# Optimization experiments

Hardware: AMD Instinct MI355X
Metric: run time of the kernel (lower is better)

## Reference

```python
import jax, jax.numpy as jnp
import numpy as np

K = 8
B = 3.0
DIM = 32
HID = 32
BATCH = 65536
MIN_BW = 1e-3
MIN_BH = 1e-3
MIN_D = 1e-3


def setup_inputs() -> dict:
    key = jax.random.key(0)
    ks = jax.random.split(key, 8)
    L = DIM - 1
    x = jax.random.normal(ks[0], (BATCH, DIM), jnp.float32)
    init_param = jax.random.uniform(ks[1], (3 * K - 1,), jnp.float32, -0.5, 0.5)
    # stacked per-dim FCNN weights; layer l conditions on x[:, :l+1] -> causal zero-mask
    w1 = jax.random.normal(ks[2], (L, L, HID), jnp.float32) * 0.2
    mask = (jnp.arange(L)[None, :] <= jnp.arange(L)[:, None]).astype(jnp.float32)
    w1 = w1 * mask[:, :, None]
    b1 = jax.random.normal(ks[3], (L, HID), jnp.float32) * 0.1
    w2 = jax.random.normal(ks[4], (L, HID, HID), jnp.float32) * 0.2
    b2 = jax.random.normal(ks[5], (L, HID), jnp.float32) * 0.1
    w3 = jax.random.normal(ks[6], (L, HID, 3 * K - 1), jnp.float32) * 0.2
    b3 = jax.random.normal(ks[7], (L, 3 * K - 1), jnp.float32) * 0.1
    return {"x": x, "init_param": init_param, "w1": w1, "b1": b1,
            "w2": w2, "b2": b2, "w3": w3, "b3": b3}


def _rqs_forward(x, Wu, Hu, Du):
    # x: [dim, batch]; Wu, Hu: [dim, batch, K]; Du: [dim, batch, K-1]
    inside = (x >= -B) & (x <= B)
    xc = jnp.clip(x, -B, B)
    # bin widths
    widths = jax.nn.softmax(Wu, axis=-1)
    widths = MIN_BW + (1.0 - MIN_BW * K) * widths
    cw = jnp.cumsum(widths, axis=-1)
    cw = jnp.concatenate([jnp.zeros(cw.shape[:-1] + (1,), cw.dtype), cw], axis=-1)
    cw = 2.0 * B * cw - B
    cw = cw.at[..., 0].set(-B).at[..., -1].set(B)
    widths = cw[..., 1:] - cw[..., :-1]
    # bin heights
    heights = jax.nn.softmax(Hu, axis=-1)
    heights = MIN_BH + (1.0 - MIN_BH * K) * heights
    ch = jnp.cumsum(heights, axis=-1)
    ch = jnp.concatenate([jnp.zeros(ch.shape[:-1] + (1,), ch.dtype), ch], axis=-1)
    ch = 2.0 * B * ch - B
    ch = ch.at[..., 0].set(-B).at[..., -1].set(B)
    heights = ch[..., 1:] - ch[..., :-1]
    # knot derivatives, edges pinned so softplus(const)+min_d = 1
    const = float(np.log(np.exp(1.0 - MIN_D) - 1.0))
    pad = jnp.full(Du.shape[:-1] + (1,), const, Du.dtype)
    derivs = MIN_D + jax.nn.softplus(jnp.concatenate([pad, Du, pad], axis=-1))  # [.., K+1]
    # bin search (searchsorted on cumwidths, eps bump on last edge)
    cw_s = cw.at[..., -1].add(1e-6)
    idx = jnp.sum((xc[..., None] >= cw_s).astype(jnp.int32), axis=-1) - 1
    idx = jnp.clip(idx, 0, K - 1)
    g = lambda a: jnp.take_along_axis(a, idx[..., None], axis=-1)[..., 0]
    in_cw = g(cw)
    in_w = g(widths)
    in_ch = g(ch)
    in_h = g(heights)
    in_delta = g(heights / widths)
    d0 = g(derivs)
    d1 = g(derivs[..., 1:])
    theta = (xc - in_cw) / in_w
    tt = theta * (1.0 - theta)
    num = in_h * (in_delta * theta ** 2 + d0 * tt)
    den = in_delta + (d0 + d1 - 2.0 * in_delta) * tt
    out = in_ch + num / den
    dnum = in_delta ** 2 * (d1 * theta ** 2 + 2.0 * in_delta * tt + d0 * (1.0 - theta) ** 2)
    ld = jnp.log(dnum) - 2.0 * jnp.log(den)
    out = jnp.where(inside, out, x)  # identity tails
    ld = jnp.where(inside, ld, 0.0)
    return out, ld


def reference(x, init_param, w1, b1, w2, b2, w3, b3):
    # all per-dim conditioners at once (w1 is causally masked in setup)
    h1 = jnp.tanh(jnp.einsum('bd,ldh->lbh', x[:, :DIM - 1], w1) + b1[:, None, :])
    h2 = jnp.tanh(jnp.einsum('lbh,lhg->lbg', h1, w2) + b2[:, None, :])
    out = jnp.einsum('lbh,lho->lbo', h2, w3) + b3[:, None, :]  # [dim-1, batch, 3K-1]
    p0 = jnp.broadcast_to(init_param, (1, x.shape[0], 3 * K - 1))
    params = jnp.concatenate([p0, out], axis=0)  # [dim, batch, 3K-1]
    Wu = 2.0 * B * jax.nn.softmax(params[..., :K], axis=-1)
    Hu = 2.0 * B * jax.nn.softmax(params[..., K:2 * K], axis=-1)
    Du = jax.nn.softplus(params[..., 2 * K:])
    z_t, ld = _rqs_forward(x.T, Wu, Hu, Du)  # [dim, batch]
    return z_t.T, jnp.sum(ld, axis=0)
```

## Files before the change

### kernel.cpp

```cpp
#include <hip/hip_runtime.h>
#include <hip/hip_bf16.h>
#include <cmath>

constexpr int KN   = 8;
constexpr int NPAR = 23;
constexpr int DD   = 32;
constexpr float BND   = 3.0f;
constexpr float MINBW = 1e-3f;
constexpr float MIND  = 1e-3f;

#define TPB   256
#define ROWS  256
#define GDIMS 4
#define WST   40
#define PSTH  24
#define RECB  8192

typedef __attribute__((ext_vector_type(8))) short short8;
typedef __attribute__((ext_vector_type(4))) float float4v;
typedef __attribute__((ext_vector_type(2))) __fp16 fp16x2;
typedef __attribute__((ext_vector_type(8))) _Float16 half8v;

#define RCP(x) __builtin_amdgcn_rcpf(x)

__device__ __forceinline__ short f2bf(float f) {
    unsigned u = __float_as_uint(f);
    u += 0x7fffu + ((u >> 16) & 1u);
    return (short)(u >> 16);
}

__device__ __forceinline__ int pkbf(float a, float b) {
    union { __hip_bfloat162 v; int i; } u;
    u.v = __float22bfloat162_rn(make_float2(a, b));
    return u.i;
}

__device__ __forceinline__ int pkh(float a, float b) {
    union { fp16x2 h; int i; } u;
    u.h = __builtin_amdgcn_cvt_pkrtz(a, b);
    return u.i;
}

__device__ __forceinline__ float fast_tanh(float x) {
    float e = __expf(2.0f * x);
    return 1.0f - 2.0f * RCP(e + 1.0f);
}

__device__ __forceinline__ float softplus_fast(float v) {
    return __logf(1.0f + __expf(v));
}

__device__ __forceinline__ float rqs_apply(float xv, const float* p, float& ldout) {
    float cw[KN + 1], ch[KN + 1];
    {
        float t0[KN]; float s = 0.f;
#pragma unroll
        for (int k = 0; k < KN; ++k) { t0[k] = __expf(p[k]); s += t0[k]; }
        float inv = (2.0f * BND) * RCP(s);
        float e2[KN]; float s2 = 0.f;
#pragma unroll
        for (int k = 0; k < KN; ++k) { e2[k] = __expf(inv * t0[k]); s2 += e2[k]; }
        float fac = (1.0f - MINBW * KN) * RCP(s2);
        float c = 0.f;
        cw[0] = -BND;
#pragma unroll
        for (int k = 0; k < KN; ++k) { c += MINBW + fac * e2[k]; cw[k + 1] = 2.0f * BND * c - BND; }
        cw[KN] = BND;
    }
    {
        float t0[KN]; float s = 0.f;
#pragma unroll
        for (int k = 0; k < KN; ++k) { t0[k] = __expf(p[KN + k]); s += t0[k]; }
        float inv = (2.0f * BND) * RCP(s);
        float e2[KN]; float s2 = 0.f;
#pragma unroll
        for (int k = 0; k < KN; ++k) { e2[k] = __expf(inv * t0[k]); s2 += e2[k]; }
        float fac = (1.0f - MINBW * KN) * RCP(s2);
        float c = 0.f;
        ch[0] = -BND;
#pragma unroll
        for (int k = 0; k < KN; ++k) { c += MINBW + fac * e2[k]; ch[k + 1] = 2.0f * BND * c - BND; }
        ch[KN] = BND;
    }

    float xc = fminf(fmaxf(xv, -BND), BND);
    float in_cw = cw[0], in_w = cw[1] - cw[0];
    float in_ch = ch[0], in_h = ch[1] - ch[0];
    float dl0 = 0.0f, dl1 = p[2 * KN];
    bool e0 = true, e1 = false;
#pragma unroll
    for (int k = 1; k < KN; ++k) {
        bool c = (xc >= cw[k]);
        in_cw = c ? cw[k]            : in_cw;
        in_w  = c ? (cw[k+1]-cw[k])  : in_w;
        in_ch = c ? ch[k]            : in_ch;
        in_h  = c ? (ch[k+1]-ch[k])  : in_h;
        dl0   = c ? p[2*KN + k - 1]  : dl0;
        if (k < KN - 1) dl1 = c ? p[2*KN + k] : dl1;
        if (k == 1)      e0 = !c;
        if (k == KN - 1) e1 = c;
    }
    float d0 = e0 ? 1.0f : (MIND + softplus_fast(softplus_fast(dl0)));
    float d1 = e1 ? 1.0f : (MIND + softplus_fast(softplus_fast(dl1)));

    float rw    = RCP(in_w);
    float th    = (xc - in_cw) * rw;
    float delta = in_h * rw;
    float tt    = th * (1.0f - th);
    float th2   = th * th;
    float num   = in_h * (delta * th2 + d0 * tt);
    float den   = delta + (d0 + d1 - 2.0f * delta) * tt;
    float z     = in_ch + num * RCP(den);
    float omt   = 1.0f - th;
    float dnum  = delta * delta * (d1 * th2 + 2.0f * delta * tt + d0 * omt * omt);
    float ldv   = __logf(dnum) - 2.0f * __logf(den);

    bool inside = (xv >= -BND) && (xv <= BND);
    ldout = inside ? ldv : 0.0f;
    return inside ? z : xv;
}

__device__ __forceinline__ short8 xpose_h(float4v cA, float4v cB,
                                          float4 bA, float4 bB,
                                          int odd, int sl_a, int sl_b, bool qlow) {
    int a0 = pkbf(fast_tanh(cA[0] + bA.x), fast_tanh(cA[1] + bA.y));
    int a1 = pkbf(fast_tanh(cA[2] + bA.z), fast_tanh(cA[3] + bA.w));
    int b0 = pkbf(fast_tanh(cB[0] + bB.x), fast_tanh(cB[1] + bB.y));
    int b1 = pkbf(fast_tanh(cB[2] + bB.z), fast_tanh(cB[3] + bB.w));
    int p0 = odd ? b0 : a0, p1 = odd ? b1 : a1;
    int p2 = odd ? a0 : b0, p3 = odd ? a1 : b1;
    int g0 = __shfl(p0, sl_a, 64);
    int g1 = __shfl(p1, sl_a, 64);
    int g2 = __shfl(p2, sl_b, 64);
    int g3 = __shfl(p3, sl_b, 64);
    union { int4 i; short8 s; } u;
    u.i = qlow ? make_int4(g0, g1, g2, g3) : make_int4(g2, g3, g0, g1);
    return u.s;
}

extern "C" __global__ void __launch_bounds__(256)
k_prep(const float* __restrict__ w1, const float* __restrict__ b1,
       const float* __restrict__ w2, const float* __restrict__ b2,
       const float* __restrict__ w3, const float* __restrict__ b3,
       char* __restrict__ wbuf, float* __restrict__ ldo, int B)
{
    const int l = blockIdx.x, tid = threadIdx.x;
    if (l >= 31) {
        const int zb = l - 31;
        const int chunk = B >> 6;
        float4* dst = (float4*)(ldo + (size_t)zb * chunk);
        for (int i = tid; i < (chunk >> 2); i += 256)
            dst[i] = make_float4(0.f, 0.f, 0.f, 0.f);
        return;
    }
    short* r1 = (short*)(wbuf + (size_t)l * RECB);
    short* r2 = r1 + 1280;
    short* r3 = r2 + 1280;
    float* f1 = (float*)(wbuf + (size_t)l * RECB + 7680);
    float* f2 = f1 + 32;
    float* f3 = f2 + 32;
    const float* g1 = w1 + (size_t)l * 992;
    const float* g2 = w2 + (size_t)l * 1024;
    const float* g3 = w3 + (size_t)l * 736;
    for (int i = tid; i < 1280; i += 256) {
        int n = i / WST, k = i - WST * n;
        r1[i] = (k < 31) ? f2bf(g1[k * 32 + n]) : (short)0;
        r2[i] = (k < 32) ? f2bf(g2[k * 32 + n]) : (short)0;
        r3[i] = (n < 23 && k < 32) ? f2bf(g3[k * 23 + n]) : (short)0;
    }
    if (tid < 32) { f1[tid] = b1[(size_t)l * 32 + tid]; f2[tid] = b2[(size_t)l * 32 + tid]; }
    if (tid < 32) f3[tid] = (tid < 23) ? b3[(size_t)l * 23 + tid] : 0.0f;
}

extern "C" __global__ void __launch_bounds__(TPB, 5)
k_nsf(const float* __restrict__ x,
      const float* __restrict__ p0,
      const char* __restrict__ wbuf,
      float* __restrict__ zo, float* __restrict__ ldo, int B)
{
    __shared__ __align__(16) char sRec[RECB];
    __shared__ __align__(16) _Float16 sP[ROWS * PSTH];

    const short* sW1 = (const short*)sRec;
    const short* sW2 = sW1 + 1280;
    const short* sW3 = sW1 + 2560;
    const float* sB1 = (const float*)(sRec + 7680);
    const float* sB2 = sB1 + 32;
    const float* sB3 = sB1 + 64;

    const int tid  = threadIdx.x;
    const int lane = tid & 63;
    const int wv   = tid >> 6;
    const int q    = lane >> 4;
    const int ln   = lane & 15;
    const int qb   = q & 1;
    const bool qlow = (q < 2);
    const int s_even = ln + 32 * qb;
    const int s_odd  = s_even + 16;
    const int sl_a = qlow ? s_even : s_odd;
    const int sl_b = qlow ? s_odd  : s_even;
    const int g    = blockIdx.y;
    const int ly0  = GDIMS * g;
    const long long rowbase = (long long)blockIdx.x * ROWS;
    const long long row = rowbase + tid;

    float xarr[GDIMS];
    {
        float4 xs = *(const float4*)(x + row * DD + ly0);
        xarr[0] = xs.x; xarr[1] = xs.y; xarr[2] = xs.z; xarr[3] = xs.w;
    }

    float zreg[GDIMS];
    float ldacc = 0.0f;

#pragma unroll
    for (int j = 0; j < GDIMS; ++j) {
        const int ly = ly0 + j;
        if (ly == 0) {
            float pr[NPAR];
#pragma unroll
            for (int k = 0; k < NPAR; ++k) pr[k] = p0[k];
            float ld;
            zreg[0] = rqs_apply(xarr[0], pr, ld);
            ldacc += ld;
            continue;
        }
        const int l = ly - 1;

        {
            const int4* src = (const int4*)(wbuf + (size_t)l * RECB);
            int4* dst = (int4*)sRec;
            dst[tid]       = src[tid];
            dst[tid + 256] = src[tid + 256];
        }
        __syncthreads();

        short8 w1a = *(const short8*)&sW1[ln * WST + q * 8];
        short8 w1b = *(const short8*)&sW1[(16 + ln) * WST + q * 8];
        short8 w2a = *(const short8*)&sW2[ln * WST + q * 8];
        short8 w2b = *(const short8*)&sW2[(16 + ln) * WST + q * 8];
        short8 w3a = *(const short8*)&sW3[ln * WST + q * 8];
        short8 w3b = *(const short8*)&sW3[(16 + ln) * WST + q * 8];
        float4 bA1 = *(const float4*)&sB1[4 * q];
        float4 bB1 = *(const float4*)&sB1[16 + 4 * q];
        float4 bA2 = *(const float4*)&sB2[4 * q];
        float4 bB2 = *(const float4*)&sB2[16 + 4 * q];
        float4 bA3 = *(const float4*)&sB3[4 * q];
        float4 bB3 = *(const float4*)&sB3[16 + 4 * q];

        short8 au[4];
#pragma unroll
        for (int t = 0; t < 4; ++t) {
            const int m0 = 64 * wv + 16 * t;
            const float4* xp = (const float4*)(x + (rowbase + m0 + ln) * DD + q * 8);
            float4 uu = xp[0], vv = xp[1];
            union { int4 i; short8 s; } c;
            c.i = make_int4(pkbf(uu.x, uu.y), pkbf(uu.z, uu.w),
                            pkbf(vv.x, vv.y), pkbf(vv.z, vv.w));
            au[t] = c.s;
        }
        float4v cA[4], cB[4];
#pragma unroll
        for (int t = 0; t < 4; ++t) {
            float4v zz = {0.f,0.f,0.f,0.f};
            cA[t] = __builtin_amdgcn_mfma_f32_16x16x32_bf16(w1a, au[t], zz, 0, 0, 0);
            cB[t] = __builtin_amdgcn_mfma_f32_16x16x32_bf16(w1b, au[t], zz, 0, 0, 0);
        }
        short8 h1f[4];
#pragma unroll
        for (int t = 0; t < 4; ++t)
            h1f[t] = xpose_h(cA[t], cB[t], bA1, bB1, qb, sl_a, sl_b, qlow);
#pragma unroll
        for (int t = 0; t < 4; ++t) {
            float4v zz = {0.f,0.f,0.f,0.f};
            cA[t] = __builtin_amdgcn_mfma_f32_16x16x32_bf16(w2a, h1f[t], zz, 0, 0, 0);
            cB[t] = __builtin_amdgcn_mfma_f32_16x16x32_bf16(w2b, h1f[t], zz, 0, 0, 0);
        }
#pragma unroll
        for (int t = 0; t < 4; ++t)
            h1f[t] = xpose_h(cA[t], cB[t], bA2, bB2, qb, sl_a, sl_b, qlow);
#pragma unroll
        for (int t = 0; t < 4; ++t) {
            float4v zz = {0.f,0.f,0.f,0.f};
            cA[t] = __builtin_amdgcn_mfma_f32_16x16x32_bf16(w3a, h1f[t], zz, 0, 0, 0);
            cB[t] = __builtin_amdgcn_mfma_f32_16x16x32_bf16(w3b, h1f[t], zz, 0, 0, 0);
        }
#pragma unroll
        for (int t = 0; t < 4; ++t) {
            const int m0 = 64 * wv + 16 * t;
            int2 pv0 = make_int2(pkh(cA[t][0] + bA3.x, cA[t][1] + bA3.y),
                                 pkh(cA[t][2] + bA3.z, cA[t][3] + bA3.w));
            *(int2*)&sP[(m0 + ln) * PSTH + 4 * q] = pv0;
            if (qlow) {
                int2 pv1 = make_int2(pkh(cB[t][0] + bB3.x, cB[t][1] + bB3.y),
                                     pkh(cB[t][2] + bB3.z, cB[t][3] + bB3.w));
                *(int2*)&sP[(m0 + ln) * PSTH + 16 + 4 * q] = pv1;
            }
        }

        {
            half8v r0 = *(const half8v*)&sP[tid * PSTH];
            half8v r1 = *(const half8v*)&sP[tid * PSTH + 8];
            half8v r2 = *(const half8v*)&sP[tid * PSTH + 16];
            float pr[NPAR];
#pragma unroll
            for (int k = 0; k < 8; ++k) pr[k] = (float)r0[k];
#pragma unroll
            for (int k = 0; k < 8; ++k) pr[8 + k] = (float)r1[k];
#pragma unroll
            for (int k = 0; k < 7; ++k) pr[16 + k] = (float)r2[k];
            float ld;
            zreg[j] = rqs_apply(xarr[j], pr, ld);
            ldacc += ld;
        }
        __syncthreads();
    }

    float4 zv = make_float4(zreg[0], zreg[1], zreg[2], zreg[3]);
    *(float4*)(zo + row * DD + ly0) = zv;
    unsafeAtomicAdd(&ldo[row], ldacc);
}

extern "C" void kernel_launch(void* const* d_in, const int* in_sizes, int n_in,
                              void* d_out, int out_size, void* d_ws, size_t ws_size,
                              hipStream_t stream) {
    const float* x  = (const float*)d_in[0];
    const float* p0 = (const float*)d_in[1];
    const float* w1 = (const float*)d_in[2];
    const float* b1 = (const float*)d_in[3];
    const float* w2 = (const float*)d_in[4];
    const float* b2 = (const float*)d_in[5];
    const float* w3 = (const float*)d_in[6];
    const float* b3 = (const float*)d_in[7];

    const int B = in_sizes[0] / DD;
    float* zo  = (float*)d_out;
    float* ldo = zo + (size_t)B * DD;
    char* wbuf = (char*)d_ws;

    hipLaunchKernelGGL(k_prep, dim3(95), dim3(256), 0, stream,
                       w1, b1, w2, b2, w3, b3, wbuf, ldo, B);
    hipLaunchKernelGGL(k_nsf, dim3(B / ROWS, DD / GDIMS), dim3(TPB), 0, stream,
                       x, p0, wbuf, zo, ldo, B);
}
```

Measured before the change: 152.0 us.

## Load MLP weights straight from global, drop block barriers, fold biases into MFMA

Each wave now reads its weight fragments and biases directly from the prepacked global buffer instead of staging them through shared memory with block-wide barriers. This removes the LDS copy and both __syncthreads per layer, since each wave only touches its own rows of the parameter scratch. The bf16 input fragments are loaded once before the layer loop instead of once per layer. Biases are passed as the MFMA accumulator init, and the parameter scratch stride is padded to 28 halves with 4-wide reads to reduce LDS bank conflicts. In exchange, the per-lane weight loads repeat in every wave and rely on L1/L2 cache hits.

```diff
diff --git a/kernel.cpp b/kernel.cpp
--- a/kernel.cpp
+++ b/kernel.cpp
@@ -13,13 +13,13 @@
 #define ROWS  256
 #define GDIMS 4
 #define WST   40
-#define PSTH  24
+#define PSTH  28
 #define RECB  8192
 
 typedef __attribute__((ext_vector_type(8))) short short8;
 typedef __attribute__((ext_vector_type(4))) float float4v;
 typedef __attribute__((ext_vector_type(2))) __fp16 fp16x2;
-typedef __attribute__((ext_vector_type(8))) _Float16 half8v;
+typedef __attribute__((ext_vector_type(4))) _Float16 half4v;
 
 #define RCP(x) __builtin_amdgcn_rcpf(x)
 
@@ -121,12 +121,11 @@
 }
 
 __device__ __forceinline__ short8 xpose_h(float4v cA, float4v cB,
-                                          float4 bA, float4 bB,
                                           int odd, int sl_a, int sl_b, bool qlow) {
-    int a0 = pkbf(fast_tanh(cA[0] + bA.x), fast_tanh(cA[1] + bA.y));
-    int a1 = pkbf(fast_tanh(cA[2] + bA.z), fast_tanh(cA[3] + bA.w));
-    int b0 = pkbf(fast_tanh(cB[0] + bB.x), fast_tanh(cB[1] + bB.y));
-    int b1 = pkbf(fast_tanh(cB[2] + bB.z), fast_tanh(cB[3] + bB.w));
+    int a0 = pkbf(fast_tanh(cA[0]), fast_tanh(cA[1]));
+    int a1 = pkbf(fast_tanh(cA[2]), fast_tanh(cA[3]));
+    int b0 = pkbf(fast_tanh(cB[0]), fast_tanh(cB[1]));
+    int b1 = pkbf(fast_tanh(cB[2]), fast_tanh(cB[3]));
     int p0 = odd ? b0 : a0, p1 = odd ? b1 : a1;
     int p2 = odd ? a0 : b0, p3 = odd ? a1 : b1;
     int g0 = __shfl(p0, sl_a, 64);
@@ -136,6 +135,10 @@
     union { int4 i; short8 s; } u;
     u.i = qlow ? make_int4(g0, g1, g2, g3) : make_int4(g2, g3, g0, g1);
     return u.s;
+}
+
+__device__ __forceinline__ float4v f4v(float4 v) {
+    float4v r; r[0] = v.x; r[1] = v.y; r[2] = v.z; r[3] = v.w; return r;
 }
 
 extern "C" __global__ void __launch_bounds__(256)
@@ -178,15 +181,7 @@
       const char* __restrict__ wbuf,
       float* __restrict__ zo, float* __restrict__ ldo, int B)
 {
-    __shared__ __align__(16) char sRec[RECB];
     __shared__ __align__(16) _Float16 sP[ROWS * PSTH];
-
-    const short* sW1 = (const short*)sRec;
-    const short* sW2 = sW1 + 1280;
-    const short* sW3 = sW1 + 2560;
-    const float* sB1 = (const float*)(sRec + 7680);
-    const float* sB2 = sB1 + 32;
-    const float* sB3 = sB1 + 64;
 
     const int tid  = threadIdx.x;
     const int lane = tid & 63;
@@ -210,6 +205,18 @@
         xarr[0] = xs.x; xarr[1] = xs.y; xarr[2] = xs.z; xarr[3] = xs.w;
     }
 
+    short8 au[4];
+#pragma unroll
+    for (int t = 0; t < 4; ++t) {
+        const int m0 = 64 * wv + 16 * t;
+        const float4* xp = (const float4*)(x + (rowbase + m0 + ln) * DD + q * 8);
+        float4 uu = xp[0], vv = xp[1];
+        union { int4 i; short8 s; } c;
+        c.i = make_int4(pkbf(uu.x, uu.y), pkbf(uu.z, uu.w),
+                        pkbf(vv.x, vv.y), pkbf(vv.z, vv.w));
+        au[t] = c.s;
+    }
+
     float zreg[GDIMS];
     float ldacc = 0.0f;
 
@@ -226,94 +233,72 @@
             continue;
         }
         const int l = ly - 1;
-
-        {
-            const int4* src = (const int4*)(wbuf + (size_t)l * RECB);
-            int4* dst = (int4*)sRec;
-            dst[tid]       = src[tid];
-            dst[tid + 256] = src[tid + 256];
-        }
-        __syncthreads();
-
-        short8 w1a = *(const short8*)&sW1[ln * WST + q * 8];
-        short8 w1b = *(const short8*)&sW1[(16 + ln) * WST + q * 8];
-        short8 w2a = *(const short8*)&sW2[ln * WST + q * 8];
-        short8 w2b = *(const short8*)&sW2[(16 + ln) * WST + q * 8];
-        short8 w3a = *(const short8*)&sW3[ln * WST + q * 8];
-        short8 w3b = *(const short8*)&sW3[(16 + ln) * WST + q * 8];
-        float4 bA1 = *(const float4*)&sB1[4 * q];
-        float4 bB1 = *(const float4*)&sB1[16 + 4 * q];
-        float4 bA2 = *(const float4*)&sB2[4 * q];
-        float4 bB2 = *(const float4*)&sB2[16 + 4 * q];
-        float4 bA3 = *(const float4*)&sB3[4 * q];
-        float4 bB3 = *(const float4*)&sB3[16 + 4 * q];
-
-        short8 au[4];
+        const char* rec = wbuf + (size_t)l * RECB;
+        const short* rw = (const short*)rec;
+        const float* rb = (const float*)(rec + 7680);
+
+        short8 w1a = *(const short8*)&rw[ln * WST + q * 8];
+        short8 w1b = *(const short8*)&rw[(16 + ln) * WST + q * 8];
+        short8 w2a = *(const short8*)&rw[1280 + ln * WST + q * 8];
+        short8 w2b = *(const short8*)&rw[1280 + (16 + ln) * WST + q * 8];
+        short8 w3a = *(const short8*)&rw[2560 + ln * WST + q * 8];
+        short8 w3b = *(const short8*)&rw[2560 + (16 + ln) * WST + q * 8];
+        float4v bA1 = f4v(*(const float4*)&rb[4 * q]);
+        float4v bB1 = f4v(*(const float4*)&rb[16 + 4 * q]);
+        float4v bA2 = f4v(*(const float4*)&rb[32 + 4 * q]);
+        float4v bB2 = f4v(*(const float4*)&rb[48 + 4 * q]);
+        float4v bA3 = f4v(*(const float4*)&rb[64 + 4 * q]);
+        float4v bB3 = f4v(*(const float4*)&rb[80 + 4 * q]);
+
+        float4v cA[4], cB[4];
+#pragma unroll
+        for (int t = 0; t < 4; ++t) {
+            cA[t] = __builtin_amdgcn_mfma_f32_16x16x32_bf16(w1a, au[t], bA1, 0, 0, 0);
+            cB[t] = __builtin_amdgcn_mfma_f32_16x16x32_bf16(w1b, au[t], bB1, 0, 0, 0);
+        }
+        short8 h1f[4];
+#pragma unroll
+        for (int t = 0; t < 4; ++t)
+            h1f[t] = xpose_h(cA[t], cB[t], qb, sl_a, sl_b, qlow);
+#pragma unroll
+        for (int t = 0; t < 4; ++t) {
+            cA[t] = __builtin_amdgcn_mfma_f32_16x16x32_bf16(w2a, h1f[t], bA2, 0, 0, 0);
+            cB[t] = __builtin_amdgcn_mfma_f32_16x16x32_bf16(w2b, h1f[t], bB2, 0, 0, 0);
+        }
+#pragma unroll
+        for (int t = 0; t < 4; ++t)
+            h1f[t] = xpose_h(cA[t], cB[t], qb, sl_a, sl_b, qlow);
+#pragma unroll
+        for (int t = 0; t < 4; ++t) {
+            cA[t] = __builtin_amdgcn_mfma_f32_16x16x32_bf16(w3a, h1f[t], bA3, 0, 0, 0);
+            cB[t] = __builtin_amdgcn_mfma_f32_16x16x32_bf16(w3b, h1f[t], bB3, 0, 0, 0);
+        }
 #pragma unroll
         for (int t = 0; t < 4; ++t) {
             const int m0 = 64 * wv + 16 * t;
-            const float4* xp = (const float4*)(x + (rowbase + m0 + ln) * DD + q * 8);
-            float4 uu = xp[0], vv = xp[1];
-            union { int4 i; short8 s; } c;
-            c.i = make_int4(pkbf(uu.x, uu.y), pkbf(uu.z, uu.w),
-                            pkbf(vv.x, vv.y), pkbf(vv.z, vv.w));
-            au[t] = c.s;
-        }
-        float4v cA[4], cB[4];
-#pragma unroll
-        for (int t = 0; t < 4; ++t) {
-            float4v zz = {0.f,0.f,0.f,0.f};
-            cA[t] = __builtin_amdgcn_mfma_f32_16x16x32_bf16(w1a, au[t], zz, 0, 0, 0);
-            cB[t] = __builtin_amdgcn_mfma_f32_16x16x32_bf16(w1b, au[t], zz, 0, 0, 0);
-        }
-        short8 h1f[4];
-#pragma unroll
-        for (int t = 0; t < 4; ++t)
-            h1f[t] = xpose_h(cA[t], cB[t], bA1, bB1, qb, sl_a, sl_b, qlow);
-#pragma unroll
-        for (int t = 0; t < 4; ++t) {
-            float4v zz = {0.f,0.f,0.f,0.f};
-            cA[t] = __builtin_amdgcn_mfma_f32_16x16x32_bf16(w2a, h1f[t], zz, 0, 0, 0);
-            cB[t] = __builtin_amdgcn_mfma_f32_16x16x32_bf16(w2b, h1f[t], zz, 0, 0, 0);
-        }
-#pragma unroll
-        for (int t = 0; t < 4; ++t)
-            h1f[t] = xpose_h(cA[t], cB[t], bA2, bB2, qb, sl_a, sl_b, qlow);
-#pragma unroll
-        for (int t = 0; t < 4; ++t) {
-            float4v zz = {0.f,0.f,0.f,0.f};
-            cA[t] = __builtin_amdgcn_mfma_f32_16x16x32_bf16(w3a, h1f[t], zz, 0, 0, 0);
-            cB[t] = __builtin_amdgcn_mfma_f32_16x16x32_bf16(w3b, h1f[t], zz, 0, 0, 0);
-        }
-#pragma unroll
-        for (int t = 0; t < 4; ++t) {
-            const int m0 = 64 * wv + 16 * t;
-            int2 pv0 = make_int2(pkh(cA[t][0] + bA3.x, cA[t][1] + bA3.y),
-                                 pkh(cA[t][2] + bA3.z, cA[t][3] + bA3.w));
+            int2 pv0 = make_int2(pkh(cA[t][0], cA[t][1]), pkh(cA[t][2], cA[t][3]));
             *(int2*)&sP[(m0 + ln) * PSTH + 4 * q] = pv0;
             if (qlow) {
-                int2 pv1 = make_int2(pkh(cB[t][0] + bB3.x, cB[t][1] + bB3.y),
-                                     pkh(cB[t][2] + bB3.z, cB[t][3] + bB3.w));
+                int2 pv1 = make_int2(pkh(cB[t][0], cB[t][1]), pkh(cB[t][2], cB[t][3]));
                 *(int2*)&sP[(m0 + ln) * PSTH + 16 + 4 * q] = pv1;
             }
         }
 
         {
-            half8v r0 = *(const half8v*)&sP[tid * PSTH];
-            half8v r1 = *(const half8v*)&sP[tid * PSTH + 8];
-            half8v r2 = *(const half8v*)&sP[tid * PSTH + 16];
-            float pr[NPAR];
-#pragma unroll
-            for (int k = 0; k < 8; ++k) pr[k] = (float)r0[k];
-#pragma unroll
-            for (int k = 0; k < 8; ++k) pr[8 + k] = (float)r1[k];
-#pragma unroll
-            for (int k = 0; k < 7; ++k) pr[16 + k] = (float)r2[k];
+            const _Float16* pp = &sP[tid * PSTH];
+            float pr[24];
+#pragma unroll
+            for (int u = 0; u < 6; ++u) {
+                half4v hv = *(const half4v*)(pp + 4 * u);
+                pr[4*u+0] = (float)hv[0];
+                pr[4*u+1] = (float)hv[1];
+                pr[4*u+2] = (float)hv[2];
+                pr[4*u+3] = (float)hv[3];
+            }
             float ld;
             zreg[j] = rqs_apply(xarr[j], pr, ld);
             ldacc += ld;
         }
-        __syncthreads();
     }
 
     float4 zv = make_float4(zreg[0], zreg[1], zreg[2], zreg[3]);
```

Measured after the change: 147.9 us. -2.7%, faster.
